# Performance work log

Measured on AMD Instinct MI355X. Metric: run time of the kernel, lower is better.

## Reference

```python
import jax, jax.numpy as jnp
import numpy as np

EPS = 1e-5  # BatchNorm2d default eps


def _conv3x3(x, w):
    # x: [B,C,H,W], w: [O,I,3,3], stride 1, 'same' padding (autopad k=3 -> p=1)
    return jax.lax.conv_general_dilated(
        x, w, window_strides=(1, 1), padding=((1, 1), (1, 1)),
        dimension_numbers=("NCHW", "OIHW", "NCHW"))


def _bn(x, g, b, m, v):
    # inference-mode BatchNorm2d with materialized running stats
    scale = (g / jnp.sqrt(v + EPS))[None, :, None, None]
    return (x - m[None, :, None, None]) * scale + b[None, :, None, None]


def _silu(x):
    return x * jax.nn.sigmoid(x)


def _pam(y, q_w, q_b, k_w, k_b, v_w, v_b, pam_gamma):
    # PAM_Module: full pixel-wise self-attention over N = H*W tokens
    B, C, H, W = y.shape
    N = H * W
    yf = y.reshape(B, C, N)
    # 1x1 convs expressed as channel matmuls; q_w: [C//8, C], v_w: [C, C]
    q = jnp.einsum("oc,bcn->bno", q_w, yf) + q_b                 # [B, N, C//8]
    k = jnp.einsum("oc,bcn->bon", k_w, yf) + k_b[None, :, None]  # [B, C//8, N]
    v = jnp.einsum("oc,bcn->bon", v_w, yf) + v_b[None, :, None]  # [B, C, N]
    energy = jnp.einsum("bno,bom->bnm", q, k)                    # [B, N, N]
    attn = jax.nn.softmax(energy, axis=-1)
    # torch: bmm(v, attn.permute(0,2,1)) -> out[b,c,n] = sum_m v[b,c,m] * attn[b,n,m]
    out = jnp.einsum("bcm,bnm->bcn", v, attn).reshape(B, C, H, W)
    return pam_gamma * out + y


def setup_inputs() -> dict:
    key = jax.random.key(0)
    ks = jax.random.split(key, 16)
    B, C1, C2, H, W = 4, 64, 64, 64, 64
    C_ = C2 // 2          # e = 0.5
    C8 = C2 // 8          # PAM q/k channels
    s = 0.05
    inp = {
        "x": jax.random.normal(ks[0], (B, C1, H, W), jnp.float32),
        # cv1: Conv(c1, c_, 3, 1)
        "cv1_w": jax.random.normal(ks[1], (C_, C1, 3, 3), jnp.float32) * s,
        "bn1_g": jax.random.uniform(ks[2], (C_,), jnp.float32, 0.5, 1.5),
        "bn1_b": jax.random.normal(ks[3], (C_,), jnp.float32) * s,
        "bn1_m": jax.random.normal(ks[4], (C_,), jnp.float32) * s,
        "bn1_v": jax.random.uniform(ks[5], (C_,), jnp.float32, 0.5, 1.5),
        # cv2: Conv(c_, c2, 3, 1)
        "cv2_w": jax.random.normal(ks[6], (C2, C_, 3, 3), jnp.float32) * s,
        "bn2_g": jax.random.uniform(ks[7], (C2,), jnp.float32, 0.5, 1.5),
        "bn2_b": jax.random.normal(ks[8], (C2,), jnp.float32) * s,
        "bn2_m": jax.random.normal(ks[9], (C2,), jnp.float32) * s,
        "bn2_v": jax.random.uniform(ks[10], (C2,), jnp.float32, 0.5, 1.5),
        # PAM 1x1 convs (flattened kernels) + biases + gamma
        "q_w": jax.random.normal(ks[11], (C8, C2), jnp.float32) * s,
        "q_b": jax.random.normal(ks[12], (C8,), jnp.float32) * s,
        "k_w": jax.random.normal(ks[13], (C8, C2), jnp.float32) * s,
        "k_b": jax.random.normal(ks[14], (C8,), jnp.float32) * s,
        "v_w": jax.random.normal(ks[15], (C2, C2), jnp.float32) * s,
        "v_b": jnp.zeros((C2,), jnp.float32),
        "pam_gamma": jnp.float32(0.5),  # torch inits 0 (identity); nonzero to exercise path
    }
    return inp


def reference(x, cv1_w, bn1_g, bn1_b, bn1_m, bn1_v,
              cv2_w, bn2_g, bn2_b, bn2_m, bn2_v,
              q_w, q_b, k_w, k_b, v_w, v_b, pam_gamma):
    y = _silu(_bn(_conv3x3(x, cv1_w), bn1_g, bn1_b, bn1_m, bn1_v))   # cv1
    y = _silu(_bn(_conv3x3(y, cv2_w), bn2_g, bn2_b, bn2_m, bn2_v))   # cv2
    # SAA: PAM applied twice on identical input and summed == 2 * PAM(y)
    att = 2.0 * _pam(y, q_w, q_b, k_w, k_b, v_w, v_b, pam_gamma)
    return x + att  # shortcut active (c1 == c2)
```

## Files before the change

kernel.cpp:

```cpp
#include <hip/hip_runtime.h>
#include <hip/hip_bf16.h>

#define NB 4
#define NN 4096

typedef short  bf16x8 __attribute__((ext_vector_type(8)));
typedef float  f32x4  __attribute__((ext_vector_type(4)));

static __device__ __forceinline__ ushort f2bf(float f) {
    unsigned u = __float_as_uint(f);
    u += 0x7fffu + ((u >> 16) & 1u);
    return (ushort)(u >> 16);
}

static __device__ __forceinline__ unsigned cvt_pk_bf16(float a, float b) {
    unsigned r;
    asm("v_cvt_pk_bf16_f32 %0, %1, %2" : "=v"(r) : "v"(a), "v"(b));
    return r;
}

__global__ __launch_bounds__(512) void conv1_mfma(
    const float* __restrict__ x, const float* __restrict__ w1,
    const float* __restrict__ bng, const float* __restrict__ bnb,
    const float* __restrict__ bnm, const float* __restrict__ bnv,
    ushort* __restrict__ y1t)
{
    __shared__ __align__(16) ushort As[32 * 600];
    __shared__ __align__(16) ushort Xs[24 * 66 * 8];

    const int tid = threadIdx.x;
    const int h = blockIdx.x, b = blockIdx.y;

    for (int cid = tid; cid < 2304; cid += 512) {
        const int row = cid / 72, off = cid % 72;
        const int k0 = off * 8;
        const int tap = k0 >> 6, ci0 = k0 & 63;
        float v[8];
        #pragma unroll
        for (int j = 0; j < 8; ++j)
            v[j] = w1[((size_t)(row * 64 + ci0 + j)) * 9 + tap];
        union { unsigned u[4]; uint4 q; } pk;
        #pragma unroll
        for (int j = 0; j < 4; ++j) pk.u[j] = cvt_pk_bf16(v[2*j], v[2*j+1]);
        *(uint4*)&As[row * 600 + off * 8] = pk.q;
    }

    {
        const int nn = tid & 63, cc = tid >> 6;
        #pragma unroll
        for (int r = 0; r < 3; ++r) {
            const int gh = h - 1 + r;
            float v[8];
            if ((unsigned)gh < 64u) {
                #pragma unroll
                for (int sub = 0; sub < 8; ++sub)
                    v[sub] = x[(((size_t)b * 64 + cc * 8 + sub) * 64 + gh) * 64 + nn];
            } else {
                #pragma unroll
                for (int sub = 0; sub < 8; ++sub) v[sub] = 0.f;
            }
            union { unsigned u[4]; uint4 q; } pk;
            #pragma unroll
            for (int j = 0; j < 4; ++j) pk.u[j] = cvt_pk_bf16(v[2*j], v[2*j+1]);
            *(uint4*)&Xs[((r * 8 + cc) * 66 + (nn + 1)) * 8] = pk.q;
        }
    }
    if (tid < 48) {
        int r = tid >> 4, q = tid & 15, cc = q >> 1, side = (q & 1) * 65;
        uint4 z = {0, 0, 0, 0};
        *(uint4*)&Xs[((r * 8 + cc) * 66 + side) * 8] = z;
    }
    __syncthreads();

    const int lane = tid & 63, wv = tid >> 6;
    const int quad = lane >> 4, l15 = lane & 15;
    const int ch = wv & 1, ph2 = wv >> 1;

    const int p = ph2 * 16 + l15;

    f32x4 acc = {0.f, 0.f, 0.f, 0.f};
    #pragma unroll
    for (int kk = 0; kk < 18; ++kk) {
        const int tap = kk >> 1;
        const int dyr = tap / 3, dx = tap % 3;
        bf16x8 af = *(const bf16x8*)&As[(ch * 16 + l15) * 600 + kk * 32 + quad * 8];
        bf16x8 bf = *(const bf16x8*)&Xs[((dyr * 8 + (kk & 1) * 4 + quad) * 66 + p + dx) * 8];
        acc = __builtin_amdgcn_mfma_f32_16x16x32_bf16(af, bf, acc, 0, 0, 0);
    }

    const int cb = ch * 16 + quad * 4;
    float r_[4];
    #pragma unroll
    for (int r = 0; r < 4; ++r) {
        int co = cb + r;
        float sc = bng[co] / sqrtf(bnv[co] + 1e-5f);
        float bs = bnb[co] - bnm[co] * sc;
        float pre = acc[r] * sc + bs;
        r_[r] = pre / (1.f + __expf(-pre));
    }
    uint2 st;
    st.x = cvt_pk_bf16(r_[0], r_[1]);
    st.y = cvt_pk_bf16(r_[2], r_[3]);
    *(uint2*)&y1t[((size_t)(b * NN + h * 64 + p)) * 32 + cb] = st;
}

__global__ __launch_bounds__(512) void conv2qkv(
    const ushort* __restrict__ y1t, const float* __restrict__ w2,
    const float* __restrict__ bng, const float* __restrict__ bnb,
    const float* __restrict__ bnm, const float* __restrict__ bnv,
    const float* __restrict__ qw, const float* __restrict__ qb,
    const float* __restrict__ kw, const float* __restrict__ kb,
    const float* __restrict__ vw, const float* __restrict__ vb,
    float* __restrict__ y, ushort* __restrict__ q8,
    ushort* __restrict__ ko, ushort* __restrict__ vt)
{
    __shared__ __align__(16) ushort As[64 * 312];
    __shared__ __align__(16) ushort Xs[12 * 66 * 8];
    __shared__ __align__(16) ushort Yt[64 * 76];
    __shared__ __align__(16) ushort Wq[80 * 76];
    __shared__ float Bv[80];

    const int tid = threadIdx.x;
    const int h = blockIdx.x, b = blockIdx.y;

    for (int cid = tid; cid < 2304; cid += 512) {
        const int row = cid / 36, off = cid % 36;
        const int k0 = off * 8;
        const int tap = k0 >> 5, ci0 = k0 & 31;
        float v[8];
        #pragma unroll
        for (int j = 0; j < 8; ++j)
            v[j] = w2[((size_t)(row * 32 + ci0 + j)) * 9 + tap];
        union { unsigned u[4]; uint4 q; } pk;
        #pragma unroll
        for (int j = 0; j < 4; ++j) pk.u[j] = cvt_pk_bf16(v[2*j], v[2*j+1]);
        *(uint4*)&As[row * 312 + off * 8] = pk.q;
    }

    for (int it = tid; it < 768; it += 512) {
        const int r = it >> 8, cid = it & 255;
        const int gh = h - 1 + r;
        const int w_ = cid >> 2, cc = cid & 3;
        uint4 v = {0, 0, 0, 0};
        if ((unsigned)gh < 64u)
            v = *(const uint4*)(y1t + ((size_t)(b * NN + gh * 64) * 32) + (size_t)cid * 8);
        *(uint4*)&Xs[((r * 4 + cc) * 66 + (w_ + 1)) * 8] = v;
    }
    if (tid < 24) {
        int r = tid >> 3, q = tid & 7, cc = q >> 1, side = (q & 1) * 65;
        uint4 z = {0, 0, 0, 0};
        *(uint4*)&Xs[((r * 4 + cc) * 66 + side) * 8] = z;
    }
    for (int i = tid; i < 2560; i += 512) {
        int chw = i >> 5, c2 = (i & 31) * 2;
        const float* src = (chw < 8) ? (qw + chw * 64 + c2)
                         : (chw < 16) ? (kw + (chw - 8) * 64 + c2)
                         : (vw + (chw - 16) * 64 + c2);
        float2 v2 = *(const float2*)src;
        *(unsigned*)&Wq[chw * 76 + c2] = cvt_pk_bf16(v2.x, v2.y);
    }
    if (tid < 80) Bv[tid] = (tid < 8) ? qb[tid] : (tid < 16) ? kb[tid - 8] : vb[tid - 16];
    __syncthreads();

    const int lane = tid & 63, wv = tid >> 6;
    const int quad = lane >> 4, l15 = lane & 15;
    const int ct2 = wv & 3, phh = wv >> 2;

    f32x4 acc[2] = {{0.f,0.f,0.f,0.f},{0.f,0.f,0.f,0.f}};
    #pragma unroll
    for (int kk = 0; kk < 9; ++kk) {
        const int dyr = kk / 3, dx = kk % 3;
        bf16x8 af = *(const bf16x8*)&As[(ct2 * 16 + l15) * 312 + kk * 32 + quad * 8];
        #pragma unroll
        for (int s = 0; s < 2; ++s) {
            int p = phh * 32 + s * 16 + l15;
            bf16x8 bf = *(const bf16x8*)&Xs[((dyr * 4 + quad) * 66 + p + dx) * 8];
            acc[s] = __builtin_amdgcn_mfma_f32_16x16x32_bf16(af, bf, acc[s], 0, 0, 0);
        }
    }

    const int cb = ct2 * 16 + quad * 4;
    float sc[4], bs[4];
    #pragma unroll
    for (int r = 0; r < 4; ++r) {
        int co = cb + r;
        sc[r] = bng[co] / sqrtf(bnv[co] + 1e-5f);
        bs[r] = bnb[co] - bnm[co] * sc[r];
    }
    #pragma unroll
    for (int s = 0; s < 2; ++s) {
        int p = phh * 32 + s * 16 + l15;
        #pragma unroll
        for (int r = 0; r < 4; ++r) {
            float pre = acc[s][r] * sc[r] + bs[r];
            float res = pre / (1.f + __expf(-pre));
            y[((size_t)(b * 64 + cb + r)) * NN + h * 64 + p] = res;
            Yt[p * 76 + cb + r] = f2bf(res);
        }
    }
    __syncthreads();

    const int pg = wv & 3;
    bf16x8 aY0 = *(const bf16x8*)&Yt[(pg * 16 + l15) * 76 + quad * 8];
    bf16x8 aY1 = *(const bf16x8*)&Yt[(pg * 16 + l15) * 76 + 32 + quad * 8];
    const int nbase = h * 64 + pg * 16 + quad * 4;
    const int vtile = h * 2 + (pg >> 1);
    const int vslot = quad * 8 + (pg & 1) * 4;
    const int cht0 = (wv < 4) ? 0 : 3;
    const int chtN = (wv < 4) ? 3 : 5;
    for (int cht = cht0; cht < chtN; ++cht) {
        bf16x8 bW0 = *(const bf16x8*)&Wq[(cht * 16 + l15) * 76 + quad * 8];
        bf16x8 bW1 = *(const bf16x8*)&Wq[(cht * 16 + l15) * 76 + 32 + quad * 8];
        f32x4 qa = {0.f, 0.f, 0.f, 0.f};
        qa = __builtin_amdgcn_mfma_f32_16x16x32_bf16(aY0, bW0, qa, 0, 0, 0);
        qa = __builtin_amdgcn_mfma_f32_16x16x32_bf16(aY1, bW1, qa, 0, 0, 0);
        const float bias = Bv[cht * 16 + l15];
        const int chn = cht * 16 + l15;
        if (cht == 0) {
            if (l15 < 8) {
                #pragma unroll
                for (int r = 0; r < 4; ++r)
                    q8[((size_t)b * NN + nbase + r) * 8 + chn] = f2bf(qa[r] + bias);
            } else {
                #pragma unroll
                for (int r = 0; r < 4; ++r)
                    ko[((size_t)b * NN + nbase + r) * 8 + (chn - 8)] = f2bf(qa[r] + bias);
            }
        } else {
            const int c = chn - 16;
            uint2 st;
            st.x = cvt_pk_bf16(qa[0] + bias, qa[1] + bias);
            st.y = cvt_pk_bf16(qa[2] + bias, qa[3] + bias);
            *(uint2*)&vt[(((size_t)(b * 128 + vtile)) * 64 + c) * 32 + vslot] = st;
        }
    }
}

__global__ __launch_bounds__(512, 2) void flash_pam(
    const ushort* __restrict__ q8,
    const ushort* __restrict__ k8,
    const ushort* __restrict__ vt,
    const float* __restrict__ y,
    const float* __restrict__ x,
    const float* __restrict__ gamma_p,
    float* __restrict__ out)
{
    __shared__ __align__(16) float Osum[4 * 4352];
    __shared__ float Lw[8][64];
    __shared__ float Ls[64];

    const int tid = threadIdx.x;
    const int bx = blockIdx.x;
    const int b  = bx >> 6;
    const int nt = bx & 63;
    const int n0 = nt * 64;

    const int lane = tid & 63, w = tid >> 6;
    const int quad = lane >> 4, l15 = lane & 15;

    const uint4 z4 = {0u, 0u, 0u, 0u};

    bf16x8 bQ[4];
    #pragma unroll
    for (int af = 0; af < 4; ++af) {
        uint4 qv = *(const uint4*)(q8 + ((size_t)b * NN + n0 + af * 16 + l15) * 8);
        uint4 sel = (quad == 0) ? qv : z4;
        bQ[af] = *(bf16x8*)&sel;
    }

    const ushort* kg = k8 + ((size_t)b * NN + w * 512) * 8;
    const ushort* vg = vt + ((size_t)(b * 128 + w * 16)) * 64 * 32;

    f32x4 acc[4][4];
    #pragma unroll
    for (int af = 0; af < 4; ++af)
        #pragma unroll
        for (int ct = 0; ct < 4; ++ct)
            acc[af][ct] = (f32x4){0.f, 0.f, 0.f, 0.f};
    float lacc[4] = {0.f, 0.f, 0.f, 0.f};
    const f32x4 zf = {0.f, 0.f, 0.f, 0.f};

    #pragma unroll 2
    for (int t = 0; t < 16; ++t) {
        const int g = t * 32;
        bf16x8 aK0 = *(const bf16x8*)(kg + (size_t)(g + l15) * 8);
        bf16x8 aK1 = *(const bf16x8*)(kg + (size_t)(g + 16 + l15) * 8);

        bf16x8 vb_[4];
        #pragma unroll
        for (int ct = 0; ct < 4; ++ct)
            vb_[ct] = *(const bf16x8*)(vg + (size_t)t * 2048 + (ct * 16 + l15) * 32 + quad * 8);

        #pragma unroll
        for (int af = 0; af < 4; ++af) {
            f32x4 s0 = __builtin_amdgcn_mfma_f32_16x16x32_bf16(aK0, bQ[af], zf, 0, 0, 0);
            f32x4 s1 = __builtin_amdgcn_mfma_f32_16x16x32_bf16(aK1, bQ[af], zf, 0, 0, 0);

            float e[8];
            #pragma unroll
            for (int r = 0; r < 4; ++r) {
                e[r]     = __expf(s0[r]);
                e[4 + r] = __expf(s1[r]);
            }
            #pragma unroll
            for (int r = 0; r < 8; ++r) lacc[af] += e[r];
            union { unsigned u[4]; bf16x8 v; } pk;
            pk.u[0] = cvt_pk_bf16(e[0], e[1]);
            pk.u[1] = cvt_pk_bf16(e[2], e[3]);
            pk.u[2] = cvt_pk_bf16(e[4], e[5]);
            pk.u[3] = cvt_pk_bf16(e[6], e[7]);

            #pragma unroll
            for (int ct = 0; ct < 4; ++ct)
                acc[af][ct] = __builtin_amdgcn_mfma_f32_16x16x32_bf16(pk.v, vb_[ct], acc[af][ct], 0, 0, 0);
        }
    }

    #pragma unroll
    for (int af = 0; af < 4; ++af) {
        lacc[af] += __shfl_xor(lacc[af], 16, 64);
        lacc[af] += __shfl_xor(lacc[af], 32, 64);
    }
    if (quad == 0) {
        #pragma unroll
        for (int af = 0; af < 4; ++af)
            Lw[w][af * 16 + l15] = lacc[af];
    }

    if (w >= 4) {
        #pragma unroll
        for (int af = 0; af < 4; ++af)
            #pragma unroll
            for (int ct = 0; ct < 4; ++ct)
                *(f32x4*)&Osum[(w - 4) * 4352 + (ct * 16 + l15) * 68 + af * 16 + quad * 4] = acc[af][ct];
    }
    __syncthreads();
    if (w < 4) {
        #pragma unroll
        for (int af = 0; af < 4; ++af)
            #pragma unroll
            for (int ct = 0; ct < 4; ++ct) {
                float* p = &Osum[w * 4352 + (ct * 16 + l15) * 68 + af * 16 + quad * 4];
                f32x4 v = *(const f32x4*)p;
                *(f32x4*)p = v + acc[af][ct];
            }
    }
    if (tid < 64) {
        float s = Lw[0][tid] + Lw[1][tid] + Lw[2][tid] + Lw[3][tid]
                + Lw[4][tid] + Lw[5][tid] + Lw[6][tid] + Lw[7][tid];
        Ls[tid] = 1.0f / s;
    }
    __syncthreads();

    {
        const int c = tid >> 3, n8 = (tid & 7) * 8;
        f32x4 o0 = {0.f, 0.f, 0.f, 0.f}, o1 = {0.f, 0.f, 0.f, 0.f};
        #pragma unroll
        for (int s = 0; s < 4; ++s) {
            o0 += *(const f32x4*)&Osum[s * 4352 + c * 68 + n8];
            o1 += *(const f32x4*)&Osum[s * 4352 + c * 68 + n8 + 4];
        }
        const float g2 = 2.f * gamma_p[0];
        const size_t idx = ((size_t)b * 64 + c) * NN + n0 + n8;
        f32x4 xv0 = *(const f32x4*)(x + idx);
        f32x4 xv1 = *(const f32x4*)(x + idx + 4);
        f32x4 yv0 = *(const f32x4*)(y + idx);
        f32x4 yv1 = *(const f32x4*)(y + idx + 4);
        f32x4 r0, r1;
        #pragma unroll
        for (int u = 0; u < 4; ++u) {
            r0[u] = xv0[u] + 2.f * yv0[u] + g2 * o0[u] * Ls[n8 + u];
            r1[u] = xv1[u] + 2.f * yv1[u] + g2 * o1[u] * Ls[n8 + 4 + u];
        }
        *(f32x4*)(out + idx) = r0;
        *(f32x4*)(out + idx + 4) = r1;
    }
}

extern "C" void kernel_launch(void* const* d_in, const int* in_sizes, int n_in,
                              void* d_out, int out_size, void* d_ws, size_t ws_size,
                              hipStream_t stream) {
    const float* x    = (const float*)d_in[0];
    const float* w1   = (const float*)d_in[1];
    const float* g1   = (const float*)d_in[2];
    const float* b1   = (const float*)d_in[3];
    const float* m1   = (const float*)d_in[4];
    const float* v1   = (const float*)d_in[5];
    const float* w2   = (const float*)d_in[6];
    const float* g2   = (const float*)d_in[7];
    const float* b2   = (const float*)d_in[8];
    const float* m2   = (const float*)d_in[9];
    const float* v2   = (const float*)d_in[10];
    const float* qw   = (const float*)d_in[11];
    const float* qb   = (const float*)d_in[12];
    const float* kw   = (const float*)d_in[13];
    const float* kb   = (const float*)d_in[14];
    const float* vw   = (const float*)d_in[15];
    const float* vb   = (const float*)d_in[16];
    const float* gam  = (const float*)d_in[17];
    float* outp = (float*)d_out;

    float* ws = (float*)d_ws;
    float*  y   = ws + 524288;
    ushort* q8  = (ushort*)(ws + 1572864);
    ushort* kk  = (ushort*)(ws + 1703936);
    ushort* vv  = (ushort*)(ws + 1769472);
    float*  S   = ws + 2326528;
    ushort* y1t = (ushort*)S;

    conv1_mfma<<<dim3(64, NB), 512, 0, stream>>>(x, w1, g1, b1, m1, v1, y1t);
    conv2qkv<<<dim3(64, NB), 512, 0, stream>>>(y1t, w2, g2, b2, m2, v2,
                                               qw, qb, kw, kb, vw, vb,
                                               y, q8, kk, vv);
    flash_pam<<<256, 512, 0, stream>>>(q8, kk, vv, y, x, gam, outp);
}
```

Measured before the change: 129.2 us.

## Fuse conv1 into conv2+QKV kernel with halo recompute of conv1 rows

Merges the conv1 kernel into the conv2/QKV kernel. Each block now recomputes the three conv1 output rows it needs (its own row plus one halo row above and below) and keeps them in registers, so the y1t intermediate no longer goes through global memory. This drops one kernel launch and the intermediate write and read, at the cost of running conv1 about three times per output row. It also adds more barriers and reuses a single union LDS buffer across the stages.

```diff
diff --git a/kernel.cpp b/kernel.cpp
--- a/kernel.cpp
+++ b/kernel.cpp
@@ -19,109 +19,111 @@
     return r;
 }
 
-__global__ __launch_bounds__(512) void conv1_mfma(
-    const float* __restrict__ x, const float* __restrict__ w1,
-    const float* __restrict__ bng, const float* __restrict__ bnb,
-    const float* __restrict__ bnm, const float* __restrict__ bnv,
-    ushort* __restrict__ y1t)
-{
-    __shared__ __align__(16) ushort As[32 * 600];
-    __shared__ __align__(16) ushort Xs[24 * 66 * 8];
-
-    const int tid = threadIdx.x;
-    const int h = blockIdx.x, b = blockIdx.y;
-
-    for (int cid = tid; cid < 2304; cid += 512) {
-        const int row = cid / 72, off = cid % 72;
-        const int k0 = off * 8;
-        const int tap = k0 >> 6, ci0 = k0 & 63;
-        float v[8];
-        #pragma unroll
-        for (int j = 0; j < 8; ++j)
-            v[j] = w1[((size_t)(row * 64 + ci0 + j)) * 9 + tap];
-        union { unsigned u[4]; uint4 q; } pk;
-        #pragma unroll
-        for (int j = 0; j < 4; ++j) pk.u[j] = cvt_pk_bf16(v[2*j], v[2*j+1]);
-        *(uint4*)&As[row * 600 + off * 8] = pk.q;
-    }
-
-    {
-        const int nn = tid & 63, cc = tid >> 6;
-        #pragma unroll
-        for (int r = 0; r < 3; ++r) {
-            const int gh = h - 1 + r;
-            float v[8];
-            if ((unsigned)gh < 64u) {
-                #pragma unroll
-                for (int sub = 0; sub < 8; ++sub)
-                    v[sub] = x[(((size_t)b * 64 + cc * 8 + sub) * 64 + gh) * 64 + nn];
-            } else {
-                #pragma unroll
-                for (int sub = 0; sub < 8; ++sub) v[sub] = 0.f;
-            }
-            union { unsigned u[4]; uint4 q; } pk;
-            #pragma unroll
-            for (int j = 0; j < 4; ++j) pk.u[j] = cvt_pk_bf16(v[2*j], v[2*j+1]);
-            *(uint4*)&Xs[((r * 8 + cc) * 66 + (nn + 1)) * 8] = pk.q;
-        }
-    }
-    if (tid < 48) {
-        int r = tid >> 4, q = tid & 15, cc = q >> 1, side = (q & 1) * 65;
-        uint4 z = {0, 0, 0, 0};
-        *(uint4*)&Xs[((r * 8 + cc) * 66 + side) * 8] = z;
-    }
-    __syncthreads();
-
-    const int lane = tid & 63, wv = tid >> 6;
-    const int quad = lane >> 4, l15 = lane & 15;
-    const int ch = wv & 1, ph2 = wv >> 1;
-
-    const int p = ph2 * 16 + l15;
-
-    f32x4 acc = {0.f, 0.f, 0.f, 0.f};
-    #pragma unroll
-    for (int kk = 0; kk < 18; ++kk) {
-        const int tap = kk >> 1;
-        const int dyr = tap / 3, dx = tap % 3;
-        bf16x8 af = *(const bf16x8*)&As[(ch * 16 + l15) * 600 + kk * 32 + quad * 8];
-        bf16x8 bf = *(const bf16x8*)&Xs[((dyr * 8 + (kk & 1) * 4 + quad) * 66 + p + dx) * 8];
-        acc = __builtin_amdgcn_mfma_f32_16x16x32_bf16(af, bf, acc, 0, 0, 0);
-    }
-
-    const int cb = ch * 16 + quad * 4;
-    float r_[4];
-    #pragma unroll
-    for (int r = 0; r < 4; ++r) {
-        int co = cb + r;
-        float sc = bng[co] / sqrtf(bnv[co] + 1e-5f);
-        float bs = bnb[co] - bnm[co] * sc;
-        float pre = acc[r] * sc + bs;
-        r_[r] = pre / (1.f + __expf(-pre));
-    }
-    uint2 st;
-    st.x = cvt_pk_bf16(r_[0], r_[1]);
-    st.y = cvt_pk_bf16(r_[2], r_[3]);
-    *(uint2*)&y1t[((size_t)(b * NN + h * 64 + p)) * 32 + cb] = st;
-}
-
-__global__ __launch_bounds__(512) void conv2qkv(
-    const ushort* __restrict__ y1t, const float* __restrict__ w2,
-    const float* __restrict__ bng, const float* __restrict__ bnb,
-    const float* __restrict__ bnm, const float* __restrict__ bnv,
+__global__ __launch_bounds__(512) void conv12qkv(
+    const float* __restrict__ x,  const float* __restrict__ w1,
+    const float* __restrict__ g1, const float* __restrict__ b1,
+    const float* __restrict__ m1, const float* __restrict__ v1,
+    const float* __restrict__ w2,
+    const float* __restrict__ g2, const float* __restrict__ b2,
+    const float* __restrict__ m2, const float* __restrict__ v2,
     const float* __restrict__ qw, const float* __restrict__ qb,
     const float* __restrict__ kw, const float* __restrict__ kb,
     const float* __restrict__ vw, const float* __restrict__ vb,
     float* __restrict__ y, ushort* __restrict__ q8,
     ushort* __restrict__ ko, ushort* __restrict__ vt)
 {
-    __shared__ __align__(16) ushort As[64 * 312];
-    __shared__ __align__(16) ushort Xs[12 * 66 * 8];
-    __shared__ __align__(16) ushort Yt[64 * 76];
-    __shared__ __align__(16) ushort Wq[80 * 76];
-    __shared__ float Bv[80];
+    __shared__ __align__(16) ushort LDSU[31872];
+    ushort* As1 = LDSU;
+    ushort* Xs1 = LDSU + 19200;
+    ushort* As2 = LDSU;
+    ushort* Xs2 = LDSU + 19968;
+    ushort* Yt  = LDSU + 26304;
+    float*  Bv  = (float*)(LDSU + 31168);
+    ushort* Wq  = LDSU;
 
     const int tid = threadIdx.x;
     const int h = blockIdx.x, b = blockIdx.y;
+
+    const int lane = tid & 63, wv = tid >> 6;
+    const int quad = lane >> 4, l15 = lane & 15;
+
+    for (int cid = tid; cid < 2304; cid += 512) {
+        const int row = cid / 72, off = cid % 72;
+        const int k0 = off * 8;
+        const int tap = k0 >> 6, ci0 = k0 & 63;
+        float v[8];
+        #pragma unroll
+        for (int j = 0; j < 8; ++j)
+            v[j] = w1[((size_t)(row * 64 + ci0 + j)) * 9 + tap];
+        union { unsigned u[4]; uint4 q; } pk;
+        #pragma unroll
+        for (int j = 0; j < 4; ++j) pk.u[j] = cvt_pk_bf16(v[2*j], v[2*j+1]);
+        *(uint4*)&As1[row * 600 + off * 8] = pk.q;
+    }
+
+    const int ch = wv & 1, ph2 = wv >> 1;
+    const int p1 = ph2 * 16 + l15;
+    const int cb1 = ch * 16 + quad * 4;
+    float sc1[4], bs1[4];
+    #pragma unroll
+    for (int r = 0; r < 4; ++r) {
+        int co = cb1 + r;
+        sc1[r] = g1[co] / sqrtf(v1[co] + 1e-5f);
+        bs1[r] = b1[co] - m1[co] * sc1[r];
+    }
+
+    uint2 yreg[3];
+    const int snn = tid & 63, scc = tid >> 6;
+    #pragma unroll
+    for (int r1 = 0; r1 < 3; ++r1) {
+        const int gh1 = h - 1 + r1;
+        #pragma unroll
+        for (int r = 0; r < 3; ++r) {
+            const int gh = gh1 - 1 + r;
+            float v[8];
+            if ((unsigned)gh < 64u) {
+                #pragma unroll
+                for (int sub = 0; sub < 8; ++sub)
+                    v[sub] = x[(((size_t)b * 64 + scc * 8 + sub) * 64 + gh) * 64 + snn];
+            } else {
+                #pragma unroll
+                for (int sub = 0; sub < 8; ++sub) v[sub] = 0.f;
+            }
+            union { unsigned u[4]; uint4 q; } pk;
+            #pragma unroll
+            for (int j = 0; j < 4; ++j) pk.u[j] = cvt_pk_bf16(v[2*j], v[2*j+1]);
+            *(uint4*)&Xs1[((r * 8 + scc) * 66 + (snn + 1)) * 8] = pk.q;
+        }
+        if (tid < 48) {
+            int r = tid >> 4, q = tid & 15, cc = q >> 1, side = (q & 1) * 65;
+            uint4 z = {0, 0, 0, 0};
+            *(uint4*)&Xs1[((r * 8 + cc) * 66 + side) * 8] = z;
+        }
+        __syncthreads();
+
+        if ((unsigned)gh1 < 64u) {
+            f32x4 acc = {0.f, 0.f, 0.f, 0.f};
+            #pragma unroll
+            for (int kk = 0; kk < 18; ++kk) {
+                const int tap = kk >> 1;
+                const int dyr = tap / 3, dx = tap % 3;
+                bf16x8 af = *(const bf16x8*)&As1[(ch * 16 + l15) * 600 + kk * 32 + quad * 8];
+                bf16x8 bf = *(const bf16x8*)&Xs1[((dyr * 8 + (kk & 1) * 4 + quad) * 66 + p1 + dx) * 8];
+                acc = __builtin_amdgcn_mfma_f32_16x16x32_bf16(af, bf, acc, 0, 0, 0);
+            }
+            float r_[4];
+            #pragma unroll
+            for (int r = 0; r < 4; ++r) {
+                float pre = acc[r] * sc1[r] + bs1[r];
+                r_[r] = pre / (1.f + __expf(-pre));
+            }
+            yreg[r1].x = cvt_pk_bf16(r_[0], r_[1]);
+            yreg[r1].y = cvt_pk_bf16(r_[2], r_[3]);
+        } else {
+            yreg[r1].x = 0u; yreg[r1].y = 0u;
+        }
+        __syncthreads();
+    }
 
     for (int cid = tid; cid < 2304; cid += 512) {
         const int row = cid / 36, off = cid % 36;
@@ -134,70 +136,62 @@
         union { unsigned u[4]; uint4 q; } pk;
         #pragma unroll
         for (int j = 0; j < 4; ++j) pk.u[j] = cvt_pk_bf16(v[2*j], v[2*j+1]);
-        *(uint4*)&As[row * 312 + off * 8] = pk.q;
-    }
-
-    for (int it = tid; it < 768; it += 512) {
-        const int r = it >> 8, cid = it & 255;
-        const int gh = h - 1 + r;
-        const int w_ = cid >> 2, cc = cid & 3;
-        uint4 v = {0, 0, 0, 0};
-        if ((unsigned)gh < 64u)
-            v = *(const uint4*)(y1t + ((size_t)(b * NN + gh * 64) * 32) + (size_t)cid * 8);
-        *(uint4*)&Xs[((r * 4 + cc) * 66 + (w_ + 1)) * 8] = v;
-    }
+        *(uint4*)&As2[row * 312 + off * 8] = pk.q;
+    }
+    #pragma unroll
+    for (int r1 = 0; r1 < 3; ++r1)
+        *(uint2*)&Xs2[((r1 * 4 + (cb1 >> 3)) * 66 + (p1 + 1)) * 8 + (cb1 & 7)] = yreg[r1];
     if (tid < 24) {
         int r = tid >> 3, q = tid & 7, cc = q >> 1, side = (q & 1) * 65;
         uint4 z = {0, 0, 0, 0};
-        *(uint4*)&Xs[((r * 4 + cc) * 66 + side) * 8] = z;
-    }
+        *(uint4*)&Xs2[((r * 4 + cc) * 66 + side) * 8] = z;
+    }
+    __syncthreads();
+
+    const int ct2 = wv & 3, phh = wv >> 2;
+    f32x4 acc2[2] = {{0.f,0.f,0.f,0.f},{0.f,0.f,0.f,0.f}};
+    #pragma unroll
+    for (int kk = 0; kk < 9; ++kk) {
+        const int dyr = kk / 3, dx = kk % 3;
+        bf16x8 af = *(const bf16x8*)&As2[(ct2 * 16 + l15) * 312 + kk * 32 + quad * 8];
+        #pragma unroll
+        for (int s = 0; s < 2; ++s) {
+            int p = phh * 32 + s * 16 + l15;
+            bf16x8 bf = *(const bf16x8*)&Xs2[((dyr * 4 + quad) * 66 + p + dx) * 8];
+            acc2[s] = __builtin_amdgcn_mfma_f32_16x16x32_bf16(af, bf, acc2[s], 0, 0, 0);
+        }
+    }
+
+    const int cb2 = ct2 * 16 + quad * 4;
+    float sc2[4], bs2[4];
+    #pragma unroll
+    for (int r = 0; r < 4; ++r) {
+        int co = cb2 + r;
+        sc2[r] = g2[co] / sqrtf(v2[co] + 1e-5f);
+        bs2[r] = b2[co] - m2[co] * sc2[r];
+    }
+    #pragma unroll
+    for (int s = 0; s < 2; ++s) {
+        int p = phh * 32 + s * 16 + l15;
+        #pragma unroll
+        for (int r = 0; r < 4; ++r) {
+            float pre = acc2[s][r] * sc2[r] + bs2[r];
+            float res = pre / (1.f + __expf(-pre));
+            y[((size_t)(b * 64 + cb2 + r)) * NN + h * 64 + p] = res;
+            Yt[p * 76 + cb2 + r] = f2bf(res);
+        }
+    }
+    __syncthreads();
+
     for (int i = tid; i < 2560; i += 512) {
         int chw = i >> 5, c2 = (i & 31) * 2;
         const float* src = (chw < 8) ? (qw + chw * 64 + c2)
                          : (chw < 16) ? (kw + (chw - 8) * 64 + c2)
                          : (vw + (chw - 16) * 64 + c2);
-        float2 v2 = *(const float2*)src;
-        *(unsigned*)&Wq[chw * 76 + c2] = cvt_pk_bf16(v2.x, v2.y);
+        float2 v2_ = *(const float2*)src;
+        *(unsigned*)&Wq[chw * 76 + c2] = cvt_pk_bf16(v2_.x, v2_.y);
     }
     if (tid < 80) Bv[tid] = (tid < 8) ? qb[tid] : (tid < 16) ? kb[tid - 8] : vb[tid - 16];
-    __syncthreads();
-
-    const int lane = tid & 63, wv = tid >> 6;
-    const int quad = lane >> 4, l15 = lane & 15;
-    const int ct2 = wv & 3, phh = wv >> 2;
-
-    f32x4 acc[2] = {{0.f,0.f,0.f,0.f},{0.f,0.f,0.f,0.f}};
-    #pragma unroll
-    for (int kk = 0; kk < 9; ++kk) {
-        const int dyr = kk / 3, dx = kk % 3;
-        bf16x8 af = *(const bf16x8*)&As[(ct2 * 16 + l15) * 312 + kk * 32 + quad * 8];
-        #pragma unroll
-        for (int s = 0; s < 2; ++s) {
-            int p = phh * 32 + s * 16 + l15;
-            bf16x8 bf = *(const bf16x8*)&Xs[((dyr * 4 + quad) * 66 + p + dx) * 8];
-            acc[s] = __builtin_amdgcn_mfma_f32_16x16x32_bf16(af, bf, acc[s], 0, 0, 0);
-        }
-    }
-
-    const int cb = ct2 * 16 + quad * 4;
-    float sc[4], bs[4];
-    #pragma unroll
-    for (int r = 0; r < 4; ++r) {
-        int co = cb + r;
-        sc[r] = bng[co] / sqrtf(bnv[co] + 1e-5f);
-        bs[r] = bnb[co] - bnm[co] * sc[r];
-    }
-    #pragma unroll
-    for (int s = 0; s < 2; ++s) {
-        int p = phh * 32 + s * 16 + l15;
-        #pragma unroll
-        for (int r = 0; r < 4; ++r) {
-            float pre = acc[s][r] * sc[r] + bs[r];
-            float res = pre / (1.f + __expf(-pre));
-            y[((size_t)(b * 64 + cb + r)) * NN + h * 64 + p] = res;
-            Yt[p * 76 + cb + r] = f2bf(res);
-        }
-    }
     __syncthreads();
 
     const int pg = wv & 3;
@@ -405,12 +399,10 @@
     ushort* q8  = (ushort*)(ws + 1572864);
     ushort* kk  = (ushort*)(ws + 1703936);
     ushort* vv  = (ushort*)(ws + 1769472);
-    float*  S   = ws + 2326528;
-    ushort* y1t = (ushort*)S;
-
-    conv1_mfma<<<dim3(64, NB), 512, 0, stream>>>(x, w1, g1, b1, m1, v1, y1t);
-    conv2qkv<<<dim3(64, NB), 512, 0, stream>>>(y1t, w2, g2, b2, m2, v2,
-                                               qw, qb, kw, kb, vw, vb,
-                                               y, q8, kk, vv);
+
+    conv12qkv<<<dim3(64, NB), 512, 0, stream>>>(x, w1, g1, b1, m1, v1,
+                                                w2, g2, b2, m2, v2,
+                                                qw, qb, kw, kb, vw, vb,
+                                                y, q8, kk, vv);
     flash_pam<<<256, 512, 0, stream>>>(q8, kk, vv, y, x, gam, outp);
 }
```

Result: no change. 130.2 us (+0.8%).
